# Optimization experiments

Hardware: AMD Instinct MI355X
Metric: run time of the kernel (lower is better)

The kernel has to match this reference:

```python
import jax, jax.numpy as jnp
import numpy as np

H = 32          # query heads
HKV = 8         # kv heads
HD = 128        # head dim
BS = 64         # sparse block size
LOCAL = 16      # local blocks
VERT = 8        # vertical stride
STEP = 1        # head sliding step = max(1, VERT // H) for non-homo heads
BASE = 1000000.0
ROPE_SCALE = 1.0
SCALE = 1.0 / np.sqrt(HD)


def setup_inputs() -> dict:
    key = jax.random.key(0)
    ks = jax.random.split(key, 6)
    T, D = 2048, H * HD
    std = 0.02
    return {
        'hidden_states': jax.random.normal(ks[0], (T, D), jnp.float32),
        'positions': jnp.arange(T, dtype=jnp.int32),
        'Wq': jax.random.normal(ks[1], (D, H * HD), jnp.float32) * std,
        'bq': jnp.zeros((H * HD,), jnp.float32),
        'Wk': jax.random.normal(ks[2], (D, HKV * HD), jnp.float32) * std,
        'bk': jnp.zeros((HKV * HD,), jnp.float32),
        'Wv': jax.random.normal(ks[3], (D, HKV * HD), jnp.float32) * std,
        'bv': jnp.zeros((HKV * HD,), jnp.float32),
        'Wo': jax.random.normal(ks[4], (D, D), jnp.float32) * std,
        'bo': jnp.zeros((D,), jnp.float32),
    }


def _rope_cos_sin(positions):
    # neox-style rotary, linear scaling (factor 1.0 -> identity)
    inv_freq = 1.0 / (BASE ** (jnp.arange(0, HD, 2, dtype=jnp.float32) / HD))  # [HD/2]
    t = positions.astype(jnp.float32) / ROPE_SCALE                             # [T]
    freqs = t[:, None] * inv_freq[None, :]                                     # [T, HD/2]
    return jnp.cos(freqs), jnp.sin(freqs)


def _apply_rope(x, cos, sin):
    # x: [T, h, HD], neox: rotate halves
    x1, x2 = x[..., : HD // 2], x[..., HD // 2 :]
    c, s = cos[:, None, :], sin[:, None, :]
    return jnp.concatenate([x1 * c - x2 * s, x2 * c + x1 * s], axis=-1)


def _block_sparse_mask(T):
    # per-head local + vertical-stride block pattern, causal at token level
    blk = jnp.arange(T) // BS
    qb, kb = blk[:, None], blk[None, :]                      # [T,T] block ids
    heads = jnp.arange(H)
    local = (qb - kb) < LOCAL                                # [T,T]
    vert = ((kb[None, :, :] + heads[:, None, None] * STEP + 1) % VERT) == 0  # [H,T,T]
    causal = jnp.arange(T)[:, None] >= jnp.arange(T)[None, :]
    return causal[None] & (local[None] | vert)               # [H,T,T] bool


def reference(hidden_states, positions, Wq, bq, Wk, bk, Wv, bv, Wo, bo):
    T = hidden_states.shape[0]
    q = (hidden_states @ Wq + bq).reshape(T, H, HD)
    k = (hidden_states @ Wk + bk).reshape(T, HKV, HD)
    v = (hidden_states @ Wv + bv).reshape(T, HKV, HD)

    cos, sin = _rope_cos_sin(positions)
    q = _apply_rope(q, cos, sin)
    k = _apply_rope(k, cos, sin)

    # GQA: repeat kv heads to match query heads
    k = jnp.repeat(k, H // HKV, axis=1)   # [T,H,HD]
    v = jnp.repeat(v, H // HKV, axis=1)

    scores = jnp.einsum('shd,thd->hst', q, k) * SCALE         # [H,T,T]
    mask = _block_sparse_mask(T)
    scores = jnp.where(mask, scores, jnp.finfo(scores.dtype).min)
    probs = jax.nn.softmax(scores, axis=-1)
    out = jnp.einsum('hst,thd->shd', probs, v).reshape(T, H * HD)
    return out @ Wo + bo
```

## Files before the change

### kernel.cpp

```cpp
#include <hip/hip_runtime.h>
#include <type_traits>

#define H_    32
#define HKV_  8
#define HD_   128
#define D_    4096
#define KVD_  1024
#define NQKV_ 6144

typedef __attribute__((ext_vector_type(8))) short s8v;
typedef __attribute__((ext_vector_type(4))) float f4v;

__device__ __forceinline__ float b2f(unsigned short u) {
  union { unsigned int i; float f; } v; v.i = ((unsigned int)u) << 16; return v.f;
}
__device__ __forceinline__ unsigned short f2b(float f) {
  unsigned int u = __float_as_uint(f);
  u += 0x7fffu + ((u >> 16) & 1u);
  return (unsigned short)(u >> 16);
}

__device__ __forceinline__ void gload16(const unsigned short* g, unsigned short* l) {
  __builtin_amdgcn_global_load_lds((const __attribute__((address_space(1))) void*)g,
                                   (__attribute__((address_space(3))) void*)l, 16, 0, 0);
}

__global__ void cvt_bf16(const float* __restrict__ x, unsigned short* __restrict__ y,
                         int n8)
{
  int i = blockIdx.x * blockDim.x + threadIdx.x;
  if (i >= n8) return;
  const float4* xp = (const float4*)x + (size_t)i * 2;
  float4 a = xp[0], b = xp[1];
  s8v v;
  v[0] = (short)f2b(a.x); v[1] = (short)f2b(a.y);
  v[2] = (short)f2b(a.z); v[3] = (short)f2b(a.w);
  v[4] = (short)f2b(b.x); v[5] = (short)f2b(b.y);
  v[6] = (short)f2b(b.z); v[7] = (short)f2b(b.w);
  *(s8v*)(y + (size_t)i * 8) = v;
}

__global__ void concat_bias(const float* __restrict__ bq, const float* __restrict__ bk,
                            const float* __restrict__ bv, float* __restrict__ o)
{
  int i = blockIdx.x * blockDim.x + threadIdx.x;
  float v = (i < D_) ? bq[i] : (i < D_ + KVD_) ? bk[i - D_] : bv[i - D_ - KVD_];
  o[i] = v;
}

__global__ __launch_bounds__(256) void cvt_transpose(
    const float* __restrict__ W, unsigned short* __restrict__ Wt, int K, int N)
{
  __shared__ unsigned short tile[64][72];
  const int k0 = blockIdx.y * 64, n0 = blockIdx.x * 64;
  const int tid = threadIdx.x;
#pragma unroll
  for (int it = 0; it < 4; ++it) {
    int idx = tid + it * 256;
    int r = idx >> 4;
    int c = (idx & 15) << 2;
    float4 w = *(const float4*)(W + (size_t)(k0 + r) * N + n0 + c);
    tile[c + 0][r] = f2b(w.x); tile[c + 1][r] = f2b(w.y);
    tile[c + 2][r] = f2b(w.z); tile[c + 3][r] = f2b(w.w);
  }
  __syncthreads();
#pragma unroll
  for (int it = 0; it < 2; ++it) {
    int idx = tid + it * 256;
    int n = idx >> 3;
    int kk = (idx & 7) << 3;
    *(s8v*)(Wt + (size_t)(n0 + n) * K + k0 + kk) = *(const s8v*)&tile[n][kk];
  }
}

__global__ __launch_bounds__(256) void vtrans(
    const unsigned short* __restrict__ S, int lds_, unsigned short* __restrict__ Dst,
    int T)
{
  __shared__ unsigned short tile[64][72];
  const int v0 = blockIdx.x * 64, t0 = blockIdx.y * 64;
  const int tid = threadIdx.x;
#pragma unroll
  for (int it = 0; it < 2; ++it) {
    int idx = tid + it * 256;
    int tr = idx >> 3;
    int vc = (idx & 7) << 3;
    s8v val = *(const s8v*)(S + (size_t)(t0 + tr) * lds_ + v0 + vc);
#pragma unroll
    for (int u = 0; u < 8; ++u) tile[vc + u][tr] = (unsigned short)val[u];
  }
  __syncthreads();
#pragma unroll
  for (int it = 0; it < 2; ++it) {
    int idx = tid + it * 256;
    int vr = idx >> 3;
    int tc = (idx & 7) << 3;
    *(s8v*)(Dst + (size_t)(v0 + vr) * T + t0 + tc) = *(const s8v*)&tile[vr][tc];
  }
}

template <typename OT>
__global__ __launch_bounds__(512, 2) void gemm_bt4p(
    const unsigned short* __restrict__ A, const unsigned short* __restrict__ Bt,
    const float* __restrict__ bias, OT* __restrict__ C,
    int M, int N, int K, int ldc)
{
  __shared__ __align__(16) unsigned short lds[65536];

  const int tid  = threadIdx.x;
  const int wave = tid >> 6;
  const int lane = tid & 63;
  const int l16  = lane & 15;
  const int quad = lane >> 4;
  const int wm   = wave >> 2;
  const int wn   = wave & 3;

  const int nbx = N >> 8;
  const int nwg = nbx * (M >> 8);
  int bid = blockIdx.x;
  if ((nwg & 7) == 0) bid = (bid & 7) * (nwg >> 3) + (bid >> 3);
  const int row0 = (bid / nbx) << 8;
  const int col0 = (bid % nbx) << 8;

  const int srow = lane >> 2;
  const int scol = (((lane & 3) ^ ((lane >> 3) & 3)) << 3);
  const unsigned short* ApL = A  + (size_t)(row0 + wave * 32 + srow) * K + scol;
  const unsigned short* BpL = Bt + (size_t)(col0 + wave * 32 + srow) * K + scol;

  unsigned short* ldsA = lds;
  unsigned short* ldsB = lds + 32768;
  const int wst = wave * 1024;

  const int sl = ((quad ^ ((l16 >> 1) & 3)) << 3);
  const int arow = wm * 128 + l16;
  const int brow = wn * 64 + l16;

  f4v acc[8][4] = {};
  const int nt = K >> 6;

  {
    const unsigned short* sa = ApL;
    const unsigned short* sb = BpL;
    gload16(sa,                       ldsA + wst);
    gload16(sa + 16 * (size_t)K,      ldsA + wst + 512);
    gload16(sb,                       ldsB + wst);
    gload16(sb + 16 * (size_t)K,      ldsB + wst + 512);
    gload16(sa + 32,                  ldsA + 8192 + wst);
    gload16(sa + 32 + 16 * (size_t)K, ldsA + 8192 + wst + 512);
    gload16(sb + 32,                  ldsB + 8192 + wst);
    gload16(sb + 32 + 16 * (size_t)K, ldsB + 8192 + wst + 512);
  }
  asm volatile("s_waitcnt vmcnt(4)" ::: "memory");
  asm volatile("s_barrier" ::: "memory");

  for (int t = 0; t < nt; ++t) {
    const int p = t & 1;
    const unsigned short* Ab0 = ldsA + p * 16384;
    const unsigned short* Ab1 = Ab0 + 8192;
    const unsigned short* Bb0 = ldsB + p * 16384;
    const unsigned short* Bb1 = Bb0 + 8192;
    unsigned short* An = ldsA + (p ^ 1) * 16384;
    unsigned short* Bn = ldsB + (p ^ 1) * 16384;
    const bool pre = (t + 1 < nt);
    const unsigned short* sa = ApL + (size_t)(t + 1) * 64;
    const unsigned short* sb = BpL + (size_t)(t + 1) * 64;

    s8v a[8], b0, b1, b2, b3;

    b0 = *(const s8v*)&Bb0[(brow +  0) * 32 + sl];
    b1 = *(const s8v*)&Bb0[(brow + 16) * 32 + sl];
#pragma unroll
    for (int i = 0; i < 8; ++i)
      a[i] = *(const s8v*)&Ab0[(arow + i * 16) * 32 + sl];
    if (pre) {
      gload16(sa,                  An + wst);
      gload16(sa + 16 * (size_t)K, An + wst + 512);
    }
    __builtin_amdgcn_s_setprio(1);
#pragma unroll
    for (int i = 0; i < 8; ++i) {
      acc[i][0] = __builtin_amdgcn_mfma_f32_16x16x32_bf16(a[i], b0, acc[i][0], 0, 0, 0);
      acc[i][1] = __builtin_amdgcn_mfma_f32_16x16x32_bf16(a[i], b1, acc[i][1], 0, 0, 0);
    }
    __builtin_amdgcn_s_setprio(0);

    b2 = *(const s8v*)&Bb0[(brow + 32) * 32 + sl];
    b3 = *(const s8v*)&Bb0[(brow + 48) * 32 + sl];
    if (pre) {
      gload16(sb,                  Bn + wst);
      gload16(sb + 16 * (size_t)K, Bn + wst + 512);
      asm volatile("s_waitcnt vmcnt(4)" ::: "memory");
    } else {
      asm volatile("s_waitcnt vmcnt(0)" ::: "memory");
    }
    asm volatile("s_barrier" ::: "memory");
    __builtin_amdgcn_s_setprio(1);
#pragma unroll
    for (int i = 0; i < 8; ++i) {
      acc[i][2] = __builtin_amdgcn_mfma_f32_16x16x32_bf16(a[i], b2, acc[i][2], 0, 0, 0);
      acc[i][3] = __builtin_amdgcn_mfma_f32_16x16x32_bf16(a[i], b3, acc[i][3], 0, 0, 0);
    }
    __builtin_amdgcn_s_setprio(0);

    b2 = *(const s8v*)&Bb1[(brow + 32) * 32 + sl];
    b3 = *(const s8v*)&Bb1[(brow + 48) * 32 + sl];
#pragma unroll
    for (int i = 0; i < 8; ++i)
      a[i] = *(const s8v*)&Ab1[(arow + i * 16) * 32 + sl];
    if (pre) {
      gload16(sa + 32,                  An + 8192 + wst);
      gload16(sa + 32 + 16 * (size_t)K, An + 8192 + wst + 512);
    }
    __builtin_amdgcn_s_setprio(1);
#pragma unroll
    for (int i = 0; i < 8; ++i) {
      acc[i][2] = __builtin_amdgcn_mfma_f32_16x16x32_bf16(a[i], b2, acc[i][2], 0, 0, 0);
      acc[i][3] = __builtin_amdgcn_mfma_f32_16x16x32_bf16(a[i], b3, acc[i][3], 0, 0, 0);
    }
    __builtin_amdgcn_s_setprio(0);

    b0 = *(const s8v*)&Bb1[(brow +  0) * 32 + sl];
    b1 = *(const s8v*)&Bb1[(brow + 16) * 32 + sl];
    if (pre) {
      gload16(sb + 32,                  Bn + 8192 + wst);
      gload16(sb + 32 + 16 * (size_t)K, Bn + 8192 + wst + 512);
      asm volatile("s_waitcnt vmcnt(4)" ::: "memory");
    }
    asm volatile("s_barrier" ::: "memory");
    __builtin_amdgcn_s_setprio(1);
#pragma unroll
    for (int i = 0; i < 8; ++i) {
      acc[i][0] = __builtin_amdgcn_mfma_f32_16x16x32_bf16(a[i], b0, acc[i][0], 0, 0, 0);
      acc[i][1] = __builtin_amdgcn_mfma_f32_16x16x32_bf16(a[i], b1, acc[i][1], 0, 0, 0);
    }
    __builtin_amdgcn_s_setprio(0);
  }

#pragma unroll
  for (int j = 0; j < 4; ++j) {
    const int col = col0 + wn * 64 + j * 16 + l16;
    const float bc = bias[col];
#pragma unroll
    for (int i = 0; i < 8; ++i) {
      const int rowb = row0 + wm * 128 + i * 16 + quad * 4;
#pragma unroll
      for (int r = 0; r < 4; ++r) {
        float o = acc[i][j][r] + bc;
        if constexpr (std::is_same_v<OT, float>) C[(size_t)(rowb + r) * ldc + col] = o;
        else                                     C[(size_t)(rowb + r) * ldc + col] = f2b(o);
      }
    }
  }
}

__global__ __launch_bounds__(512, 1) void gemm_o2(
    const unsigned short* __restrict__ A, const unsigned short* __restrict__ Bt,
    const float* __restrict__ bias, float* __restrict__ C,
    int M, int N, int K)
{
  __shared__ __align__(16) unsigned short lds[49152];

  const int tid  = threadIdx.x;
  const int wave = tid >> 6;
  const int lane = tid & 63;
  const int l16  = lane & 15;
  const int quad = lane >> 4;
  const int wm   = wave >> 2;
  const int wn   = wave & 3;

  const int nbx = N >> 8;
  const int nwg = nbx * (M >> 7);
  int bid = blockIdx.x;
  if ((nwg & 7) == 0) bid = (bid & 7) * (nwg >> 3) + (bid >> 3);
  const int row0 = (bid / nbx) << 7;
  const int col0 = (bid % nbx) << 8;

  const int srow = lane >> 2;
  const int scol = (((lane & 3) ^ ((lane >> 3) & 3)) << 3);
  const unsigned short* ApL = A  + (size_t)(row0 + wave * 16 + srow) * K + scol;
  const unsigned short* BpL = Bt + (size_t)(col0 + wave * 32 + srow) * K + scol;

  unsigned short* ldsA = lds;
  unsigned short* ldsB = lds + 16384;
  const int wstA = wave * 512;
  const int wstB = wave * 1024;

  const int sl = ((quad ^ ((l16 >> 1) & 3)) << 3);
  const int arow = wm * 64 + l16;
  const int brow = wn * 64 + l16;

  f4v acc[4][4] = {};
  const int nt = K >> 6;

  gload16(ApL,                       ldsA + wstA);
  gload16(BpL,                       ldsB + wstB);
  gload16(BpL + 16 * (size_t)K,      ldsB + wstB + 512);
  gload16(ApL + 32,                  ldsA + 4096 + wstA);
  gload16(BpL + 32,                  ldsB + 8192 + wstB);
  gload16(BpL + 32 + 16 * (size_t)K, ldsB + 8192 + wstB + 512);
  asm volatile("s_waitcnt vmcnt(3)" ::: "memory");
  asm volatile("s_barrier" ::: "memory");

  for (int t = 0; t < nt; ++t) {
    const int p = t & 1;
    const unsigned short* Ab0 = ldsA + p * 8192;
    const unsigned short* Ab1 = Ab0 + 4096;
    const unsigned short* Bb0 = ldsB + p * 16384;
    const unsigned short* Bb1 = Bb0 + 8192;
    unsigned short* An = ldsA + (p ^ 1) * 8192;
    unsigned short* Bn = ldsB + (p ^ 1) * 16384;
    const bool pre = (t + 1 < nt);
    const unsigned short* sa = ApL + (size_t)(t + 1) * 64;
    const unsigned short* sb = BpL + (size_t)(t + 1) * 64;

    s8v a[4], b[4];

#pragma unroll
    for (int i = 0; i < 4; ++i)
      a[i] = *(const s8v*)&Ab0[(arow + i * 16) * 32 + sl];
#pragma unroll
    for (int j = 0; j < 4; ++j)
      b[j] = *(const s8v*)&Bb0[(brow + j * 16) * 32 + sl];
    if (pre) {
      gload16(sa,                  An + wstA);
      gload16(sb,                  Bn + wstB);
      gload16(sb + 16 * (size_t)K, Bn + wstB + 512);
    }
    __builtin_amdgcn_s_setprio(1);
#pragma unroll
    for (int i = 0; i < 4; ++i)
#pragma unroll
      for (int j = 0; j < 4; ++j)
        acc[i][j] = __builtin_amdgcn_mfma_f32_16x16x32_bf16(a[i], b[j], acc[i][j], 0, 0, 0);
    __builtin_amdgcn_s_setprio(0);
    if (pre) { asm volatile("s_waitcnt vmcnt(3)" ::: "memory"); }
    else     { asm volatile("s_waitcnt vmcnt(0)" ::: "memory"); }
    asm volatile("s_barrier" ::: "memory");

#pragma unroll
    for (int i = 0; i < 4; ++i)
      a[i] = *(const s8v*)&Ab1[(arow + i * 16) * 32 + sl];
#pragma unroll
    for (int j = 0; j < 4; ++j)
      b[j] = *(const s8v*)&Bb1[(brow + j * 16) * 32 + sl];
    if (pre) {
      gload16(sa + 32,                  An + 4096 + wstA);
      gload16(sb + 32,                  Bn + 8192 + wstB);
      gload16(sb + 32 + 16 * (size_t)K, Bn + 8192 + wstB + 512);
    }
    __builtin_amdgcn_s_setprio(1);
#pragma unroll
    for (int i = 0; i < 4; ++i)
#pragma unroll
      for (int j = 0; j < 4; ++j)
        acc[i][j] = __builtin_amdgcn_mfma_f32_16x16x32_bf16(a[i], b[j], acc[i][j], 0, 0, 0);
    __builtin_amdgcn_s_setprio(0);
    if (pre) { asm volatile("s_waitcnt vmcnt(3)" ::: "memory"); }
    asm volatile("s_barrier" ::: "memory");
  }

#pragma unroll
  for (int j = 0; j < 4; ++j) {
    const int col = col0 + wn * 64 + j * 16 + l16;
    const float bc = bias[col];
#pragma unroll
    for (int i = 0; i < 4; ++i) {
      const int rowb = row0 + wm * 64 + i * 16 + quad * 4;
#pragma unroll
      for (int r = 0; r < 4; ++r)
        C[(size_t)(rowb + r) * N + col] = acc[i][j][r] + bc;
    }
  }
}

__global__ void sincos_tab(const int* __restrict__ pos, float* __restrict__ ct,
                           float* __restrict__ st)
{
  const int t = blockIdx.x, d = threadIdx.x;
  float inv = powf(1.0e6f, -(float)d * (1.0f / 64.0f));
  float fr  = (float)pos[t] * inv;
  float s, c;
  sincosf(fr, &s, &c);
  ct[t * 64 + d] = c;
  st[t * 64 + d] = s;
}

__global__ __launch_bounds__(320) void rope_apply2(
    unsigned short* __restrict__ qkv,
    const float* __restrict__ ct, const float* __restrict__ st, int T)
{
  const int t   = blockIdx.x;
  const int tid = threadIdx.x;
  const int hh  = tid >> 3;
  const int d0  = (tid & 7) << 3;
  unsigned short* p = qkv + (size_t)t * NQKV_ + hh * HD_;
  const float g = (hh < H_) ? (0.08838834764831845f * 1.4426950408889634f) : 1.0f;

  s8v x1 = *(const s8v*)(p + d0);
  s8v x2 = *(const s8v*)(p + 64 + d0);
  const float4* cp = (const float4*)(ct + t * 64 + d0);
  const float4* sp = (const float4*)(st + t * 64 + d0);
  float4 ca = cp[0], cb = cp[1], sa = sp[0], sb = sp[1];
  float cc[8] = {ca.x, ca.y, ca.z, ca.w, cb.x, cb.y, cb.z, cb.w};
  float ss[8] = {sa.x, sa.y, sa.z, sa.w, sb.x, sb.y, sb.z, sb.w};

  s8v o1, o2;
#pragma unroll
  for (int u = 0; u < 8; ++u) {
    float a = b2f((unsigned short)x1[u]);
    float b = b2f((unsigned short)x2[u]);
    o1[u] = (short)f2b((a * cc[u] - b * ss[u]) * g);
    o2[u] = (short)f2b((b * cc[u] + a * ss[u]) * g);
  }
  *(s8v*)(p + d0)      = o1;
  *(s8v*)(p + 64 + d0) = o2;
}

__global__ __launch_bounds__(256) void attn_sparse(
    const unsigned short* __restrict__ QKV, int ldq,
    const unsigned short* __restrict__ Vt, unsigned short* __restrict__ O, int T)
{
  __shared__ __align__(16) unsigned short lds[16384];
  unsigned short* ldsK = lds;
  unsigned short* ldsV = lds + 8192;
  unsigned short* ldsP = lds;

  const int h    = blockIdx.x;
  const int qb   = (gridDim.y - 1) - blockIdx.y;
  const int hkv  = h >> 2;
  const int tid  = threadIdx.x;
  const int wave = tid >> 6;
  const int lane = tid & 63;
  const int l16  = lane & 15;
  const int quad = lane >> 4;

  const int qrow = qb * 64 + wave * 16 + l16;
  s8v qf[4];
#pragma unroll
  for (int s = 0; s < 4; ++s)
    qf[s] = *(const s8v*)(QKV + (size_t)qrow * ldq + h * HD_ + s * 32 + quad * 8);

  const int lr4 = lane >> 2;
  const int lc8 = (lane & 3) << 3;
  const unsigned short* Kp0 = QKV + (size_t)(wave * 16 + lr4) * ldq
                              + D_ + hkv * HD_ + lc8;
  unsigned short* Kd0 = ldsK + wave * 512;
  const unsigned short* Vp0 = Vt + (size_t)(hkv * HD_ + wave * 32 + lr4) * T + lc8;
  unsigned short* Vd0 = ldsV + wave * 1024;

  float mrow[4] = {-1e30f, -1e30f, -1e30f, -1e30f};
  float lrow[4] = {0.f, 0.f, 0.f, 0.f};
  f4v oacc[8] = {};
  const int rowinb = wave * 16 + quad * 4;

  for (int kb = 0; kb <= qb; ++kb) {
    if (!((qb - kb < 16) || (((kb + h + 1) & 7) == 0))) continue;

    __syncthreads();
    {
      const unsigned short* kp = Kp0 + (size_t)(kb * 64) * ldq;
      const unsigned short* vp = Vp0 + kb * 64;
#pragma unroll
      for (int t = 0; t < 4; ++t)
        gload16(kp + t * 32, Kd0 + t * 2048);
#pragma unroll
      for (int t = 0; t < 4; ++t)
        gload16(vp + (size_t)((t >> 1) * 16) * T + (t & 1) * 32,
                Vd0 + (t & 1) * 4096 + (t >> 1) * 512);
    }
    __syncthreads();

    f4v sacc[4] = {};
#pragma unroll
    for (int kt = 0; kt < 4; ++kt) {
#pragma unroll
      for (int s = 0; s < 4; ++s) {
        s8v b = *(const s8v*)&ldsK[s * 2048 + (kt * 16 + l16) * 32 + quad * 8];
        sacc[kt] = __builtin_amdgcn_mfma_f32_16x16x32_bf16(qf[s], b, sacc[kt], 0, 0, 0);
      }
    }
    __syncthreads();

    const bool diag = (kb == qb);
    float p[4][4];
#pragma unroll
    for (int r = 0; r < 4; ++r) {
      float mx = -1e30f;
#pragma unroll
      for (int kt = 0; kt < 4; ++kt) {
        float sc = sacc[kt][r];
        if (diag && (kt * 16 + l16 > rowinb + r)) sc = -1e30f;
        p[r][kt] = sc;
        mx = fmaxf(mx, sc);
      }
#pragma unroll
      for (int off = 1; off < 16; off <<= 1)
        mx = fmaxf(mx, __shfl_xor(mx, off));
      float newm = fmaxf(mrow[r], mx);
      float alpha = exp2f(mrow[r] - newm);
      mrow[r] = newm;
      float rs = 0.f;
#pragma unroll
      for (int kt = 0; kt < 4; ++kt) {
        unsigned short pb = f2b(exp2f(p[r][kt] - newm));
        ldsP[wave * 1152 + (quad * 4 + r) * 72 + kt * 16 + l16] = pb;
        rs += b2f(pb);
      }
#pragma unroll
      for (int off = 1; off < 16; off <<= 1)
        rs += __shfl_xor(rs, off);
      lrow[r] = lrow[r] * alpha + rs;
#pragma unroll
      for (int dt = 0; dt < 8; ++dt) oacc[dt][r] *= alpha;
    }

#pragma unroll
    for (int s2 = 0; s2 < 2; ++s2) {
      s8v af = *(const s8v*)&ldsP[wave * 1152 + l16 * 72 + s2 * 32 + quad * 8];
#pragma unroll
      for (int dt = 0; dt < 8; ++dt) {
        s8v vf = *(const s8v*)&ldsV[s2 * 4096 + (dt * 16 + l16) * 32 + quad * 8];
        oacc[dt] = __builtin_amdgcn_mfma_f32_16x16x32_bf16(af, vf, oacc[dt], 0, 0, 0);
      }
    }
  }

#pragma unroll
  for (int r = 0; r < 4; ++r) {
    float inv = 1.0f / lrow[r];
    size_t rowoff = (size_t)(qb * 64 + rowinb + r) * D_ + h * HD_;
#pragma unroll
    for (int dt = 0; dt < 8; ++dt)
      O[rowoff + dt * 16 + l16] = f2b(oacc[dt][r] * inv);
  }
}

extern "C" void kernel_launch(void* const* d_in, const int* in_sizes, int n_in,
                              void* d_out, int out_size, void* d_ws, size_t ws_size,
                              hipStream_t stream)
{
  const float* hs  = (const float*)d_in[0];
  const int*   pos = (const int*)d_in[1];
  const float* Wq  = (const float*)d_in[2];
  const float* bq  = (const float*)d_in[3];
  const float* Wk  = (const float*)d_in[4];
  const float* bk  = (const float*)d_in[5];
  const float* Wv  = (const float*)d_in[6];
  const float* bv  = (const float*)d_in[7];
  const float* Wo  = (const float*)d_in[8];
  const float* bo  = (const float*)d_in[9];
  float* out = (float*)d_out;

  const int T = in_sizes[1];

  const size_t nQ = (size_t)T * D_;
  unsigned short* hsb  = (unsigned short*)d_ws;
  unsigned short* qkv  = hsb + nQ;
  unsigned short* vt   = qkv + (size_t)T * NQKV_;
  unsigned short* wbuf = vt  + (size_t)KVD_ * T;
  unsigned short* tail = wbuf + (size_t)NQKV_ * D_;
  float* bqkv = (float*)tail;
  float* ct   = bqkv + NQKV_;
  float* st   = ct + (size_t)T * 64;
  unsigned short* abuf = hsb;

  dim3 blk(256);
  cvt_bf16<<<dim3((int)(nQ / 8 / 256)), blk, 0, stream>>>(hs, hsb, (int)(nQ / 8));
  concat_bias<<<dim3(NQKV_ / 256), blk, 0, stream>>>(bq, bk, bv, bqkv);
  sincos_tab<<<dim3(T), dim3(64), 0, stream>>>(pos, ct, st);

  cvt_transpose<<<dim3(D_ / 64,   D_ / 64), blk, 0, stream>>>(Wq, wbuf, D_, D_);
  cvt_transpose<<<dim3(KVD_ / 64, D_ / 64), blk, 0, stream>>>(
      Wk, wbuf + (size_t)D_ * D_, D_, KVD_);
  cvt_transpose<<<dim3(KVD_ / 64, D_ / 64), blk, 0, stream>>>(
      Wv, wbuf + (size_t)(D_ + KVD_) * D_, D_, KVD_);

  gemm_bt4p<unsigned short><<<dim3((NQKV_ / 256) * (T / 256)), dim3(512), 0, stream>>>(
      hsb, wbuf, bqkv, qkv, T, NQKV_, D_, NQKV_);

  rope_apply2<<<dim3(T), dim3(320), 0, stream>>>(qkv, ct, st, T);
  vtrans<<<dim3(KVD_ / 64, T / 64), blk, 0, stream>>>(
      qkv + D_ + KVD_, NQKV_, vt, T);

  attn_sparse<<<dim3(H_, T / 64), blk, 0, stream>>>(qkv, NQKV_, vt, abuf, T);

  cvt_transpose<<<dim3(D_ / 64, D_ / 64), blk, 0, stream>>>(Wo, wbuf, D_, D_);
  gemm_o2<<<dim3((D_ / 256) * (T / 128)), dim3(512), 0, stream>>>(
      abuf, wbuf, bo, out, T, D_, D_);
}
```

Baseline: 491.8 us.

## Retile QKV GEMM to 256x192 tiles so the grid fills all CUs

Replaces the 256x256-tile QKV projection GEMM with a 256x192-tile variant, raising the workgroup count from 192 to 256 to match the CU count. The LDS staging and load schedule are reorganized to use three B sub-loads per K-tile, and the inner loop is simplified to two barrier phases per 64-wide K step. Per-wave output shrinks and the arithmetic intensity per tile drops slightly, and occupancy hints change to one block per CU.

```diff
diff --git a/kernel.cpp b/kernel.cpp
--- a/kernel.cpp
+++ b/kernel.cpp
@@ -99,13 +99,12 @@
   }
 }
 
-template <typename OT>
-__global__ __launch_bounds__(512, 2) void gemm_bt4p(
+__global__ __launch_bounds__(512, 1) void gemm_q192(
     const unsigned short* __restrict__ A, const unsigned short* __restrict__ Bt,
-    const float* __restrict__ bias, OT* __restrict__ C,
+    const float* __restrict__ bias, unsigned short* __restrict__ C,
     int M, int N, int K, int ldc)
 {
-  __shared__ __align__(16) unsigned short lds[65536];
+  __shared__ __align__(16) unsigned short lds[57344];
 
   const int tid  = threadIdx.x;
   const int wave = tid >> 6;
@@ -115,140 +114,117 @@
   const int wm   = wave >> 2;
   const int wn   = wave & 3;
 
-  const int nbx = N >> 8;
+  const int nbx = N / 192;
   const int nwg = nbx * (M >> 8);
   int bid = blockIdx.x;
   if ((nwg & 7) == 0) bid = (bid & 7) * (nwg >> 3) + (bid >> 3);
   const int row0 = (bid / nbx) << 8;
-  const int col0 = (bid % nbx) << 8;
-
-  const int srow = lane >> 2;
+  const int col0 = (bid % nbx) * 192;
+
+  const int srow = wave * 16 + (lane >> 2);
   const int scol = (((lane & 3) ^ ((lane >> 3) & 3)) << 3);
-  const unsigned short* ApL = A  + (size_t)(row0 + wave * 32 + srow) * K + scol;
-  const unsigned short* BpL = Bt + (size_t)(col0 + wave * 32 + srow) * K + scol;
+  const unsigned short* ApL = A + (size_t)(row0 + srow) * K + scol;
+  const unsigned short* Bp0;
+  const unsigned short* Bp1;
+  const unsigned short* Bp2;
+  {
+    int R0 = srow;
+    int R1 = 128 + srow;
+    int R2 = 256 + srow;
+    int kh1r = (R1 >= 192);
+    Bp0 = Bt + (size_t)(col0 + R0) * K + scol;
+    Bp1 = Bt + (size_t)(col0 + (R1 - kh1r * 192)) * K + kh1r * 32 + scol;
+    Bp2 = Bt + (size_t)(col0 + (R2 - 192)) * K + 32 + scol;
+  }
 
   unsigned short* ldsA = lds;
   unsigned short* ldsB = lds + 32768;
-  const int wst = wave * 1024;
+  const int wsl = wave * 512;
 
   const int sl = ((quad ^ ((l16 >> 1) & 3)) << 3);
   const int arow = wm * 128 + l16;
-  const int brow = wn * 64 + l16;
-
-  f4v acc[8][4] = {};
+  const int brow = wn * 48 + l16;
+
+  f4v acc[8][3] = {};
   const int nt = K >> 6;
 
-  {
-    const unsigned short* sa = ApL;
-    const unsigned short* sb = BpL;
-    gload16(sa,                       ldsA + wst);
-    gload16(sa + 16 * (size_t)K,      ldsA + wst + 512);
-    gload16(sb,                       ldsB + wst);
-    gload16(sb + 16 * (size_t)K,      ldsB + wst + 512);
-    gload16(sa + 32,                  ldsA + 8192 + wst);
-    gload16(sa + 32 + 16 * (size_t)K, ldsA + 8192 + wst + 512);
-    gload16(sb + 32,                  ldsB + 8192 + wst);
-    gload16(sb + 32 + 16 * (size_t)K, ldsB + 8192 + wst + 512);
-  }
-  asm volatile("s_waitcnt vmcnt(4)" ::: "memory");
+  gload16(ApL,                        ldsA + wsl);
+  gload16(ApL + (size_t)128 * K,      ldsA + 4096 + wsl);
+  gload16(Bp0,                        ldsB + wsl);
+  gload16(Bp1,                        ldsB + 4096 + wsl);
+  gload16(ApL + 32,                   ldsA + 8192 + wsl);
+  gload16(ApL + 32 + (size_t)128 * K, ldsA + 12288 + wsl);
+  gload16(Bp2,                        ldsB + 8192 + wsl);
+  asm volatile("s_waitcnt vmcnt(3)" ::: "memory");
   asm volatile("s_barrier" ::: "memory");
 
   for (int t = 0; t < nt; ++t) {
     const int p = t & 1;
     const unsigned short* Ab0 = ldsA + p * 16384;
     const unsigned short* Ab1 = Ab0 + 8192;
-    const unsigned short* Bb0 = ldsB + p * 16384;
-    const unsigned short* Bb1 = Bb0 + 8192;
+    const unsigned short* Bb  = ldsB + p * 12288;
     unsigned short* An = ldsA + (p ^ 1) * 16384;
-    unsigned short* Bn = ldsB + (p ^ 1) * 16384;
+    unsigned short* Bn = ldsB + (p ^ 1) * 12288;
     const bool pre = (t + 1 < nt);
-    const unsigned short* sa = ApL + (size_t)(t + 1) * 64;
-    const unsigned short* sb = BpL + (size_t)(t + 1) * 64;
-
-    s8v a[8], b0, b1, b2, b3;
-
-    b0 = *(const s8v*)&Bb0[(brow +  0) * 32 + sl];
-    b1 = *(const s8v*)&Bb0[(brow + 16) * 32 + sl];
+    const size_t adv = (size_t)(t + 1) * 64;
+
+    s8v a[8], b[3];
+
 #pragma unroll
     for (int i = 0; i < 8; ++i)
       a[i] = *(const s8v*)&Ab0[(arow + i * 16) * 32 + sl];
+#pragma unroll
+    for (int j = 0; j < 3; ++j)
+      b[j] = *(const s8v*)&Bb[(brow + j * 16) * 32 + sl];
     if (pre) {
-      gload16(sa,                  An + wst);
-      gload16(sa + 16 * (size_t)K, An + wst + 512);
+      gload16(ApL + adv,                   An + wsl);
+      gload16(ApL + adv + (size_t)128 * K, An + 4096 + wsl);
+      gload16(Bp0 + adv,                   Bn + wsl);
     }
     __builtin_amdgcn_s_setprio(1);
 #pragma unroll
-    for (int i = 0; i < 8; ++i) {
-      acc[i][0] = __builtin_amdgcn_mfma_f32_16x16x32_bf16(a[i], b0, acc[i][0], 0, 0, 0);
-      acc[i][1] = __builtin_amdgcn_mfma_f32_16x16x32_bf16(a[i], b1, acc[i][1], 0, 0, 0);
-    }
+    for (int i = 0; i < 8; ++i)
+#pragma unroll
+      for (int j = 0; j < 3; ++j)
+        acc[i][j] = __builtin_amdgcn_mfma_f32_16x16x32_bf16(a[i], b[j], acc[i][j], 0, 0, 0);
     __builtin_amdgcn_s_setprio(0);
-
-    b2 = *(const s8v*)&Bb0[(brow + 32) * 32 + sl];
-    b3 = *(const s8v*)&Bb0[(brow + 48) * 32 + sl];
-    if (pre) {
-      gload16(sb,                  Bn + wst);
-      gload16(sb + 16 * (size_t)K, Bn + wst + 512);
-      asm volatile("s_waitcnt vmcnt(4)" ::: "memory");
-    } else {
-      asm volatile("s_waitcnt vmcnt(0)" ::: "memory");
-    }
+    if (pre) { asm volatile("s_waitcnt vmcnt(3)" ::: "memory"); }
+    else     { asm volatile("s_waitcnt vmcnt(0)" ::: "memory"); }
     asm volatile("s_barrier" ::: "memory");
-    __builtin_amdgcn_s_setprio(1);
-#pragma unroll
-    for (int i = 0; i < 8; ++i) {
-      acc[i][2] = __builtin_amdgcn_mfma_f32_16x16x32_bf16(a[i], b2, acc[i][2], 0, 0, 0);
-      acc[i][3] = __builtin_amdgcn_mfma_f32_16x16x32_bf16(a[i], b3, acc[i][3], 0, 0, 0);
-    }
-    __builtin_amdgcn_s_setprio(0);
-
-    b2 = *(const s8v*)&Bb1[(brow + 32) * 32 + sl];
-    b3 = *(const s8v*)&Bb1[(brow + 48) * 32 + sl];
+
 #pragma unroll
     for (int i = 0; i < 8; ++i)
       a[i] = *(const s8v*)&Ab1[(arow + i * 16) * 32 + sl];
+#pragma unroll
+    for (int j = 0; j < 3; ++j)
+      b[j] = *(const s8v*)&Bb[6144 + (brow + j * 16) * 32 + sl];
     if (pre) {
-      gload16(sa + 32,                  An + 8192 + wst);
-      gload16(sa + 32 + 16 * (size_t)K, An + 8192 + wst + 512);
+      gload16(Bp1 + adv,                        Bn + 4096 + wsl);
+      gload16(ApL + adv + 32,                   An + 8192 + wsl);
+      gload16(ApL + adv + 32 + (size_t)128 * K, An + 12288 + wsl);
+      gload16(Bp2 + adv,                        Bn + 8192 + wsl);
     }
     __builtin_amdgcn_s_setprio(1);
 #pragma unroll
-    for (int i = 0; i < 8; ++i) {
-      acc[i][2] = __builtin_amdgcn_mfma_f32_16x16x32_bf16(a[i], b2, acc[i][2], 0, 0, 0);
-      acc[i][3] = __builtin_amdgcn_mfma_f32_16x16x32_bf16(a[i], b3, acc[i][3], 0, 0, 0);
-    }
+    for (int i = 0; i < 8; ++i)
+#pragma unroll
+      for (int j = 0; j < 3; ++j)
+        acc[i][j] = __builtin_amdgcn_mfma_f32_16x16x32_bf16(a[i], b[j], acc[i][j], 0, 0, 0);
     __builtin_amdgcn_s_setprio(0);
-
-    b0 = *(const s8v*)&Bb1[(brow +  0) * 32 + sl];
-    b1 = *(const s8v*)&Bb1[(brow + 16) * 32 + sl];
-    if (pre) {
-      gload16(sb + 32,                  Bn + 8192 + wst);
-      gload16(sb + 32 + 16 * (size_t)K, Bn + 8192 + wst + 512);
-      asm volatile("s_waitcnt vmcnt(4)" ::: "memory");
-    }
+    if (pre) { asm volatile("s_waitcnt vmcnt(3)" ::: "memory"); }
     asm volatile("s_barrier" ::: "memory");
-    __builtin_amdgcn_s_setprio(1);
-#pragma unroll
-    for (int i = 0; i < 8; ++i) {
-      acc[i][0] = __builtin_amdgcn_mfma_f32_16x16x32_bf16(a[i], b0, acc[i][0], 0, 0, 0);
-      acc[i][1] = __builtin_amdgcn_mfma_f32_16x16x32_bf16(a[i], b1, acc[i][1], 0, 0, 0);
-    }
-    __builtin_amdgcn_s_setprio(0);
-  }
-
-#pragma unroll
-  for (int j = 0; j < 4; ++j) {
-    const int col = col0 + wn * 64 + j * 16 + l16;
+  }
+
+#pragma unroll
+  for (int j = 0; j < 3; ++j) {
+    const int col = col0 + wn * 48 + j * 16 + l16;
     const float bc = bias[col];
 #pragma unroll
     for (int i = 0; i < 8; ++i) {
       const int rowb = row0 + wm * 128 + i * 16 + quad * 4;
 #pragma unroll
-      for (int r = 0; r < 4; ++r) {
-        float o = acc[i][j][r] + bc;
-        if constexpr (std::is_same_v<OT, float>) C[(size_t)(rowb + r) * ldc + col] = o;
-        else                                     C[(size_t)(rowb + r) * ldc + col] = f2b(o);
-      }
+      for (int r = 0; r < 4; ++r)
+        C[(size_t)(rowb + r) * ldc + col] = f2b(acc[i][j][r] + bc);
     }
   }
 }
@@ -575,7 +551,7 @@
   cvt_transpose<<<dim3(KVD_ / 64, D_ / 64), blk, 0, stream>>>(
       Wv, wbuf + (size_t)(D_ + KVD_) * D_, D_, KVD_);
 
-  gemm_bt4p<unsigned short><<<dim3((NQKV_ / 256) * (T / 256)), dim3(512), 0, stream>>>(
+  gemm_q192<<<dim3((NQKV_ / 192) * (T / 256)), dim3(512), 0, stream>>>(
       hsb, wbuf, bqkv, qkv, T, NQKV_, D_, NQKV_);
 
   rope_apply2<<<dim3(T), dim3(320), 0, stream>>>(qkv, ct, st, T);
```

Result: no change. 501.1 us (+1.9%).
